# Performance work log

Measured on AMD Instinct MI355X. Metric: run time of the kernel, lower is better.

The kernel has to match this reference:

```python
import jax, jax.numpy as jnp
import numpy as np

H = 256          # hidden_channels
NP, NJ, NC = 8192, 8192, 4096  # person / job_posting / company node counts
EA, EW, EP = 262144, 131072, 131072  # edge counts per relation


def _gcn(x_src, W, b, edge_index, num_src, num_dst):
    """Bipartite GCNConv: h = x_src @ W; out[dst] = sum_e norm_e * h[src_e] + b,
    norm = deg_out(src)^-1/2 * deg_in(dst)^-1/2 (symmetric GCN normalization)."""
    h = x_src @ W                                # [num_src, H]
    row, col = edge_index[0], edge_index[1]
    ones = jnp.ones(row.shape[0], dtype=h.dtype)
    deg_src = jax.ops.segment_sum(ones, row, num_segments=num_src)
    deg_dst = jax.ops.segment_sum(ones, col, num_segments=num_dst)
    dis_src = jnp.where(deg_src > 0, jax.lax.rsqrt(jnp.maximum(deg_src, 1e-12)), 0.0)
    dis_dst = jnp.where(deg_dst > 0, jax.lax.rsqrt(jnp.maximum(deg_dst, 1e-12)), 0.0)
    norm = dis_src[row] * dis_dst[col]           # [E]
    out = jax.ops.segment_sum(h[row] * norm[:, None], col, num_segments=num_dst)
    return out + b


def setup_inputs() -> dict:
    key = jax.random.key(0)
    ks = jax.random.split(key, 12)
    s = 1.0 / np.sqrt(H)
    return {
        "x_person":  jax.random.normal(ks[0], (NP, H), jnp.float32),
        "x_job":     jax.random.normal(ks[1], (NJ, H), jnp.float32),
        "x_company": jax.random.normal(ks[2], (NC, H), jnp.float32),
        "ei_applied": jax.random.randint(ks[3], (2, EA), 0, 8192, jnp.int64 if jax.config.read('jax_enable_x64') else jnp.int32),
        "ei_worked":  jax.random.randint(ks[4], (2, EW), 0, 4096, jnp.int64 if jax.config.read('jax_enable_x64') else jnp.int32),
        "ei_posted":  jax.random.randint(ks[5], (2, EP), 0, 4096, jnp.int64 if jax.config.read('jax_enable_x64') else jnp.int32),
        "W_aj": jax.random.normal(ks[6], (H, H), jnp.float32) * s,
        "b_aj": jnp.zeros((H,), jnp.float32),
        "W_wa": jax.random.normal(ks[7], (H, H), jnp.float32) * s,
        "b_wa": jnp.zeros((H,), jnp.float32),
        "W_pb": jax.random.normal(ks[8], (H, H), jnp.float32) * s,
        "b_pb": jnp.zeros((H,), jnp.float32),
    }


def reference(x_person, x_job, x_company, ei_applied, ei_worked, ei_posted,
              W_aj, b_aj, W_wa, b_wa, W_pb, b_pb):
    Np, Nj, Nc = x_person.shape[0], x_job.shape[0], x_company.shape[0]
    # HeteroConv with aggr='sum': each dst type sums messages over its edge types
    job_emb = _gcn(x_person, W_aj, b_aj, ei_applied, Np, Nj)
    comp_emb = (_gcn(x_person, W_wa, b_wa, ei_worked, Np, Nc)
                + _gcn(x_job, W_pb, b_pb, ei_posted, Nj, Nc))  # computed but unused downstream
    del comp_emb
    person_emb = x_person  # 'person' is never a dst type; features pass through
    scores = jax.nn.sigmoid(person_emb @ job_emb.T)  # [Np, Nj]
    return scores
```

## Files before the change

kernel.cpp:

```cpp
#include <hip/hip_runtime.h>
#include <hip/hip_bf16.h>

#define HCH 256
#define NPN 8192
#define NJN 8192
#define EAE 262144

typedef _Float16 f16x8 __attribute__((ext_vector_type(8)));
typedef _Float16 f16x4 __attribute__((ext_vector_type(4)));
typedef _Float16 f16x2 __attribute__((ext_vector_type(2)));
typedef float f32x4 __attribute__((ext_vector_type(4)));

typedef __attribute__((address_space(1))) void glb_void;
typedef __attribute__((address_space(3))) void lds_void;

#define WS_DEG_SRC   0
#define WS_DEG_DST   32768
#define WS_CUR       65536
#define WS_OFFS      98304
#define WS_DIS_SRC   131328
#define WS_DIS_DST   164096
#define WS_CSR       196864
#define WS_XH        1245440
#define WS_ZH        5439744
#define WS_GH        9634048
#define WS_WHT       13828352

__global__ void k_zero(int* p) {
    int i = blockIdx.x * 256 + threadIdx.x;
    p[i] = 0;
}

__global__ void k_count(const int* __restrict__ row, const int* __restrict__ col,
                        int* deg_src, int* deg_dst) {
    int e = blockIdx.x * 256 + threadIdx.x;
    if (e < EAE) {
        atomicAdd(&deg_src[row[e]], 1);
        atomicAdd(&deg_dst[col[e]], 1);
    }
}

__global__ void k_prep(const int* __restrict__ deg_src, const int* __restrict__ deg_dst,
                       int* __restrict__ offs, float* __restrict__ dis_src,
                       float* __restrict__ dis_dst, const float* __restrict__ W,
                       _Float16* __restrict__ WhT, const float* __restrict__ x,
                       _Float16* __restrict__ Xh) {
    int bid = blockIdx.x;
    int t = threadIdx.x;
    if (bid == 0) {
        __shared__ int part[256];
        int base = t * 32;
        int local[32];
        int s = 0;
#pragma unroll
        for (int i = 0; i < 32; i++) { local[i] = s; s += deg_dst[base + i]; }
        part[t] = s;
        __syncthreads();
        for (int d = 1; d < 256; d <<= 1) {
            int self = part[t];
            int add = (t >= d) ? part[t - d] : 0;
            __syncthreads();
            part[t] = self + add;
            __syncthreads();
        }
        int chunk_excl = (t > 0) ? part[t - 1] : 0;
#pragma unroll
        for (int i = 0; i < 32; i++) offs[base + i] = chunk_excl + local[i];
        if (t == 255) offs[NJN] = part[255];
    } else if (bid < 65) {
        int i = (bid - 1) * 256 + t;
        if (i < NPN) {
            int d = deg_src[i];
            dis_src[i] = d > 0 ? rsqrtf((float)d) : 0.f;
        } else {
            int j = i - NPN;
            int d = deg_dst[j];
            dis_dst[j] = d > 0 ? rsqrtf((float)d) : 0.f;
        }
    } else if (bid < 321) {
        int idx = (bid - 65) * 256 + t;
        int n = idx >> 8, k = idx & 255;
        WhT[idx] = (_Float16)W[k * HCH + n];
    } else {
        int i = ((bid - 321) * 256 + t) * 4;
        float4 v = *(const float4*)(x + i);
        f16x4 h;
        h[0] = (_Float16)v.x; h[1] = (_Float16)v.y;
        h[2] = (_Float16)v.z; h[3] = (_Float16)v.w;
        *(f16x4*)(Xh + i) = h;
    }
}

__global__ void k_bucket(const int* __restrict__ row, const int* __restrict__ col,
                         const int* __restrict__ offs, int* cur, int* csr) {
    int e = blockIdx.x * 256 + threadIdx.x;
    if (e < EAE) {
        int c = col[e];
        int p = atomicAdd(&cur[c], 1);
        csr[offs[c] + p] = row[e];
    }
}

__global__ void k_agg(const _Float16* __restrict__ Xh, const int* __restrict__ csr,
                      const int* __restrict__ offs, const float* __restrict__ dis_src,
                      const float* __restrict__ dis_dst, _Float16* __restrict__ Zh) {
    int j = blockIdx.x;
    int c = threadIdx.x;
    int e0 = offs[j], e1 = offs[j + 1];
    float a0 = 0.f, a1 = 0.f;
    int e = e0;
    for (; e + 1 < e1; e += 2) {
        int s0 = csr[e], s1 = csr[e + 1];
        float w0 = dis_src[s0], w1 = dis_src[s1];
        f16x2 v0 = *(const f16x2*)(Xh + (size_t)s0 * HCH + 2 * c);
        f16x2 v1 = *(const f16x2*)(Xh + (size_t)s1 * HCH + 2 * c);
        a0 += w0 * (float)v0[0] + w1 * (float)v1[0];
        a1 += w0 * (float)v0[1] + w1 * (float)v1[1];
    }
    if (e < e1) {
        int s0 = csr[e];
        float w0 = dis_src[s0];
        f16x2 v0 = *(const f16x2*)(Xh + (size_t)s0 * HCH + 2 * c);
        a0 += w0 * (float)v0[0];
        a1 += w0 * (float)v0[1];
    }
    float dd = dis_dst[j];
    f16x2 out;
    out[0] = (_Float16)(a0 * dd);
    out[1] = (_Float16)(a1 * dd);
    *(f16x2*)(Zh + (size_t)j * HCH + 2 * c) = out;
}

template <int TM, int TN, bool SIGMOID>
__global__ __launch_bounds__(256, 2)
void k_gemm(const _Float16* __restrict__ A, const _Float16* __restrict__ Bt,
            const float* __restrict__ bias, void* __restrict__ Cout, int Ncols) {
    constexpr int WM = TM / 2, WN = TN / 2;
    constexpr int MR = WM / 16, NR = WN / 16;
    constexpr int CHA = TM * 8 / 256;
    constexpr int CHB = TN * 8 / 256;
    constexpr int BOFF = TM * 128;

    __shared__ _Float16 sm[2][(TM + TN) * 64];

    int tid = threadIdx.x;
    int wid = tid >> 6, lane = tid & 63;

    int bx = blockIdx.x, by = blockIdx.y;
    if (SIGMOID) {
        int nbx = gridDim.x;
        int lin = by * nbx + bx;
        int chunk = (nbx * gridDim.y) >> 3;
        int swz = (lin & 7) * chunk + (lin >> 3);
        bx = swz % nbx;
        by = swz / nbx;
    }
    int brow = by * TM;
    int bcol = bx * TN;
    int wrow = (wid >> 1) * WM;
    int wcol = (wid & 1) * WN;

    f32x4 acc[MR][NR] = {};

    int lr = lane & 15;
    int kq = lane >> 4;

    auto stage = [&](int t, int b) {
        int k0 = t * 64;
#pragma unroll
        for (int i = 0; i < CHA; i++) {
            int wc0 = i * 256 + wid * 64;
            int c = wc0 + lane;
            int r = c >> 3, cc = c & 7;
            const char* ga = (const char*)A +
                (size_t)(brow + r) * (HCH * 2) + (size_t)(k0 + cc * 8) * 2;
            __builtin_amdgcn_global_load_lds(
                (glb_void*)ga, (lds_void*)((char*)sm[b] + wc0 * 16), 16, 0, 0);
        }
#pragma unroll
        for (int i = 0; i < CHB; i++) {
            int wc0 = i * 256 + wid * 64;
            int c = wc0 + lane;
            int r = c >> 3, cc = c & 7;
            const char* gb = (const char*)Bt +
                (size_t)(bcol + r) * (HCH * 2) + (size_t)(k0 + cc * 8) * 2;
            __builtin_amdgcn_global_load_lds(
                (glb_void*)gb, (lds_void*)((char*)sm[b] + BOFF + wc0 * 16), 16, 0, 0);
        }
    };

    stage(0, 0);
    __syncthreads();

    constexpr int NT = HCH / 64;
#pragma unroll
    for (int t = 0; t < NT; t++) {
        int cur = t & 1;
        if (t + 1 < NT) stage(t + 1, cur ^ 1);
        const char* base = (const char*)sm[cur];
#pragma unroll
        for (int kk = 0; kk < 64; kk += 32) {
            f16x8 af[MR], bfr[NR];
            int kbyte = (kk + kq * 8) * 2;
#pragma unroll
            for (int m = 0; m < MR; m++) {
                int r = wrow + m * 16 + lr;
                af[m] = *(const f16x8*)(base + r * 128 + kbyte);
            }
#pragma unroll
            for (int n = 0; n < NR; n++) {
                int r = wcol + n * 16 + lr;
                bfr[n] = *(const f16x8*)(base + BOFF + r * 128 + kbyte);
            }
#pragma unroll
            for (int m = 0; m < MR; m++)
#pragma unroll
                for (int n = 0; n < NR; n++)
                    acc[m][n] = __builtin_amdgcn_mfma_f32_16x16x32_f16(
                        af[m], bfr[n], acc[m][n], 0, 0, 0);
        }
        __syncthreads();
    }

    int rq = lane >> 4;
#pragma unroll
    for (int m = 0; m < MR; m++) {
#pragma unroll
        for (int n = 0; n < NR; n++) {
#pragma unroll
            for (int j = 0; j < 4; j++) {
                int gr = brow + wrow + m * 16 + rq * 4 + j;
                int gc = bcol + wcol + n * 16 + lr;
                float v = acc[m][n][j];
                if (SIGMOID) {
                    float e = __expf(-v);
                    ((float*)Cout)[(size_t)gr * Ncols + gc] =
                        __builtin_amdgcn_rcpf(1.f + e);
                } else {
                    v += bias[gc];
                    ((_Float16*)Cout)[(size_t)gr * Ncols + gc] = (_Float16)v;
                }
            }
        }
    }
}

extern "C" void kernel_launch(void* const* d_in, const int* in_sizes, int n_in,
                              void* d_out, int out_size, void* d_ws, size_t ws_size,
                              hipStream_t stream) {
    const float* x_person = (const float*)d_in[0];
    const int*   ei_app   = (const int*)d_in[3];
    const float* W_aj     = (const float*)d_in[6];
    const float* b_aj     = (const float*)d_in[7];

    const int* erow = ei_app;
    const int* ecol = ei_app + EAE;

    char* w = (char*)d_ws;
    int*   deg_src = (int*)(w + WS_DEG_SRC);
    int*   deg_dst = (int*)(w + WS_DEG_DST);
    int*   cur     = (int*)(w + WS_CUR);
    int*   offs    = (int*)(w + WS_OFFS);
    float* dis_src = (float*)(w + WS_DIS_SRC);
    float* dis_dst = (float*)(w + WS_DIS_DST);
    int*   csr     = (int*)(w + WS_CSR);
    _Float16* Xh   = (_Float16*)(w + WS_XH);
    _Float16* Zh   = (_Float16*)(w + WS_ZH);
    _Float16* Gh   = (_Float16*)(w + WS_GH);
    _Float16* WhT  = (_Float16*)(w + WS_WHT);

    k_zero<<<96, 256, 0, stream>>>((int*)w);
    k_count<<<EAE / 256, 256, 0, stream>>>(erow, ecol, deg_src, deg_dst);
    k_prep<<<2369, 256, 0, stream>>>(deg_src, deg_dst, offs, dis_src, dis_dst,
                                     W_aj, WhT, x_person, Xh);
    k_bucket<<<EAE / 256, 256, 0, stream>>>(erow, ecol, offs, cur, csr);
    k_agg<<<NJN, 128, 0, stream>>>(Xh, csr, offs, dis_src, dis_dst, Zh);
    {
        dim3 grid(HCH / 128, NJN / 64);
        k_gemm<64, 128, false><<<grid, 256, 0, stream>>>(Zh, WhT, b_aj, (void*)Gh, HCH);
    }
    {
        dim3 grid(NJN / 128, NPN / 128);
        k_gemm<128, 128, true><<<grid, 256, 0, stream>>>(Xh, Gh, nullptr, d_out, NJN);
    }
}
```

Baseline: 156.8 us.

## Add persistent A-resident GEMM for score matrix with XCD-aware strip mapping

Replaces the tiled 128x128 score GEMM with a persistent kernel of 256 blocks of 512 threads. Each block keeps a 128-row strip of person features (full K=256) resident in swizzled LDS and sweeps 32 column tiles of 64 job embeddings, double-buffering the B tiles. Block IDs are mapped so blocks on the same XCD share column groups, aiming for L2 reuse of B. The intent is to remove repeated A reloads and the K loop, at the cost of smaller per-wave tiles, one block per CU, and a sync per column tile.

```diff
diff --git a/kernel.cpp b/kernel.cpp
--- a/kernel.cpp
+++ b/kernel.cpp
@@ -131,10 +131,10 @@
     *(f16x2*)(Zh + (size_t)j * HCH + 2 * c) = out;
 }
 
-template <int TM, int TN, bool SIGMOID>
+template <int TM, int TN>
 __global__ __launch_bounds__(256, 2)
 void k_gemm(const _Float16* __restrict__ A, const _Float16* __restrict__ Bt,
-            const float* __restrict__ bias, void* __restrict__ Cout, int Ncols) {
+            const float* __restrict__ bias, _Float16* __restrict__ Cout, int Ncols) {
     constexpr int WM = TM / 2, WN = TN / 2;
     constexpr int MR = WM / 16, NR = WN / 16;
     constexpr int CHA = TM * 8 / 256;
@@ -146,17 +146,8 @@
     int tid = threadIdx.x;
     int wid = tid >> 6, lane = tid & 63;
 
-    int bx = blockIdx.x, by = blockIdx.y;
-    if (SIGMOID) {
-        int nbx = gridDim.x;
-        int lin = by * nbx + bx;
-        int chunk = (nbx * gridDim.y) >> 3;
-        int swz = (lin & 7) * chunk + (lin >> 3);
-        bx = swz % nbx;
-        by = swz / nbx;
-    }
-    int brow = by * TM;
-    int bcol = bx * TN;
+    int brow = blockIdx.y * TM;
+    int bcol = blockIdx.x * TN;
     int wrow = (wid >> 1) * WM;
     int wcol = (wid & 1) * WN;
 
@@ -231,17 +222,103 @@
             for (int j = 0; j < 4; j++) {
                 int gr = brow + wrow + m * 16 + rq * 4 + j;
                 int gc = bcol + wcol + n * 16 + lr;
-                float v = acc[m][n][j];
-                if (SIGMOID) {
+                float v = acc[m][n][j] + bias[gc];
+                Cout[(size_t)gr * Ncols + gc] = (_Float16)v;
+            }
+        }
+    }
+}
+
+#define G2_NW 32
+__global__ __launch_bounds__(512, 1)
+void k_gemm2(const _Float16* __restrict__ A, const _Float16* __restrict__ Bt,
+             float* __restrict__ C) {
+    __shared__ _Float16 smA[128 * HCH];
+    __shared__ _Float16 smB[2][64 * HCH];
+
+    int tid = threadIdx.x;
+    int wid = tid >> 6, lane = tid & 63;
+    int lr = lane & 15, kq = lane >> 4;
+
+    int id = blockIdx.x;
+    int xcd = id & 7, slot = id >> 3;
+    int cg = xcd >> 1;
+    int strip = slot + (xcd & 1) * 32;
+    int brow = strip * 128;
+    int bcol0 = cg * (64 * G2_NW);
+
+    int wrow = (wid >> 1) * 32;
+    int wcol = (wid & 1) * 32;
+
+#pragma unroll
+    for (int i = 0; i < 8; i++) {
+        int wc0 = i * 512 + wid * 64;
+        int c = wc0 + lane;
+        int r = c >> 5, q = c & 31;
+        int j = q ^ (r & 7);
+        const char* ga = (const char*)(A + (size_t)(brow + r) * HCH + j * 8);
+        __builtin_amdgcn_global_load_lds(
+            (glb_void*)ga, (lds_void*)((char*)smA + wc0 * 16), 16, 0, 0);
+    }
+    auto stageB = [&](int t, int b) {
+#pragma unroll
+        for (int i = 0; i < 4; i++) {
+            int wc0 = i * 512 + wid * 64;
+            int c = wc0 + lane;
+            int r = c >> 5, q = c & 31;
+            int j = q ^ (r & 7);
+            const char* gb = (const char*)(Bt +
+                (size_t)(bcol0 + t * 64 + r) * HCH + j * 8);
+            __builtin_amdgcn_global_load_lds(
+                (glb_void*)gb, (lds_void*)((char*)smB[b] + wc0 * 16), 16, 0, 0);
+        }
+    };
+    stageB(0, 0);
+    __syncthreads();
+
+    for (int t = 0; t < G2_NW; t++) {
+        int cb = t & 1;
+        if (t + 1 < G2_NW) stageB(t + 1, cb ^ 1);
+        const char* sA = (const char*)smA;
+        const char* sB = (const char*)smB[cb];
+        f32x4 acc[2][2] = {};
+#pragma unroll
+        for (int ks = 0; ks < 8; ks++) {
+            f16x8 af[2], bf2[2];
+            int sb = ks * 4 + kq;
+#pragma unroll
+            for (int m = 0; m < 2; m++) {
+                int r = wrow + m * 16 + lr;
+                af[m] = *(const f16x8*)(sA + r * 512 + ((sb ^ (r & 7)) << 4));
+            }
+#pragma unroll
+            for (int n = 0; n < 2; n++) {
+                int r = wcol + n * 16 + lr;
+                bf2[n] = *(const f16x8*)(sB + r * 512 + ((sb ^ (r & 7)) << 4));
+            }
+#pragma unroll
+            for (int m = 0; m < 2; m++)
+#pragma unroll
+                for (int n = 0; n < 2; n++)
+                    acc[m][n] = __builtin_amdgcn_mfma_f32_16x16x32_f16(
+                        af[m], bf2[n], acc[m][n], 0, 0, 0);
+        }
+        int bcol = bcol0 + t * 64;
+#pragma unroll
+        for (int m = 0; m < 2; m++) {
+#pragma unroll
+            for (int n = 0; n < 2; n++) {
+#pragma unroll
+                for (int j = 0; j < 4; j++) {
+                    int gr = brow + wrow + m * 16 + kq * 4 + j;
+                    int gc = bcol + wcol + n * 16 + lr;
+                    float v = acc[m][n][j];
                     float e = __expf(-v);
-                    ((float*)Cout)[(size_t)gr * Ncols + gc] =
-                        __builtin_amdgcn_rcpf(1.f + e);
-                } else {
-                    v += bias[gc];
-                    ((_Float16*)Cout)[(size_t)gr * Ncols + gc] = (_Float16)v;
+                    C[(size_t)gr * NJN + gc] = __builtin_amdgcn_rcpf(1.f + e);
                 }
             }
         }
+        __syncthreads();
     }
 }
 
@@ -277,10 +354,7 @@
     k_agg<<<NJN, 128, 0, stream>>>(Xh, csr, offs, dis_src, dis_dst, Zh);
     {
         dim3 grid(HCH / 128, NJN / 64);
-        k_gemm<64, 128, false><<<grid, 256, 0, stream>>>(Zh, WhT, b_aj, (void*)Gh, HCH);
-    }
-    {
-        dim3 grid(NJN / 128, NPN / 128);
-        k_gemm<128, 128, true><<<grid, 256, 0, stream>>>(Xh, Gh, nullptr, d_out, NJN);
-    }
-}
+        k_gemm<64, 128><<<grid, 256, 0, stream>>>(Zh, WhT, b_aj, Gh, HCH);
+    }
+    k_gemm2<<<256, 512, 0, stream>>>(Xh, Gh, (float*)d_out);
+}
```

Result: faster. 153.6 us (-2.0%).
